# Kernel tuning notes

Hardware: AMD Instinct MI355X
Metric: run time of the kernel (lower is better)

Reference implementation:

```python
import jax, jax.numpy as jnp
import numpy as np

N = 100000   # nodes
E = 1600000  # edges (avg degree 16)
F_IN, F_HID, F_OUT = 64, 64, 16


def setup_inputs() -> dict:
    key = jax.random.key(0)
    ks = jax.random.split(key, 10)
    features = jax.random.normal(ks[0], (N, F_IN), dtype=jnp.float32)
    src = jax.random.randint(ks[1], (E,), 0, N, dtype=jnp.int32)
    dst = jax.random.randint(ks[2], (E,), 0, N, dtype=jnp.int32)
    # Xavier-uniform weights, zero bias (matches nn.init in the module)
    def xavier(k, fan_in, fan_out):
        lim = np.sqrt(6.0 / (fan_in + fan_out))
        return jax.random.uniform(k, (fan_in, fan_out), jnp.float32, -lim, lim)
    return {
        "features": features,
        "W1": xavier(ks[3], F_IN, F_HID), "b1": jnp.zeros((F_HID,), jnp.float32),
        "W2": xavier(ks[4], F_HID, F_HID), "b2": jnp.zeros((F_HID,), jnp.float32),
        "W3": xavier(ks[5], F_HID, F_OUT), "b3": jnp.zeros((F_OUT,), jnp.float32),
        "src": src, "dst": dst,
    }


def pairnorm_scs(x):
    # PairNorm 'PN-SCS', scale=1
    col_mean = x.mean(axis=0)                                    # [F]
    rownorm = jnp.sqrt(1e-6 + jnp.sum(x * x, axis=1, keepdims=True))  # [N,1]
    return x / rownorm - col_mean


def graph_conv(h, src, dst, W, b):
    # copy_u('h','m') + sum reduce over edges, plus self-loop
    agg = jax.ops.segment_sum(h[src], dst, num_segments=N) + h   # [N,F]
    return agg @ W + b


def reference(features, W1, b1, W2, b2, W3, b3, src, dst):
    h = features
    for W, b in ((W1, b1), (W2, b2)):
        h = pairnorm_scs(h)
        h = jax.nn.relu(graph_conv(h, src, dst, W, b))
        # dropout p=0.0 -> identity
    return graph_conv(h, src, dst, W3, b3)
```

## Files before the change

### kernel.cpp

```cpp
#include <hip/hip_runtime.h>
#include <hip/hip_fp8.h>


#define NHB 128

typedef float floatx2 __attribute__((ext_vector_type(2)));

__device__ __forceinline__ unsigned short f2bf(float f) {
  unsigned u = __builtin_bit_cast(unsigned, f);
  u += 0x7FFFu + ((u >> 16) & 1u);
  return (unsigned short)(u >> 16);
}
__device__ __forceinline__ float bf2f(unsigned short h) {
  return __builtin_bit_cast(float, ((unsigned)h) << 16);
}
__device__ __forceinline__ float rlane(float v, int k) {
  return __builtin_bit_cast(
      float, __builtin_amdgcn_readlane(__builtin_bit_cast(int, v), k));
}
__device__ __forceinline__ unsigned char f2fp8(float f) {
  __hip_fp8_e4m3 t(f);
  return (unsigned char)t.__x;
}
__device__ __forceinline__ float fp8tof(unsigned v) {
#if __has_builtin(__builtin_amdgcn_cvt_f32_fp8)
  return __builtin_amdgcn_cvt_f32_fp8((int)v, 0);
#else
  const unsigned h = ((v << 8) & 0x8000u) | ((v << 7) & 0x3f80u);
  __half_raw hr; hr.x = (unsigned short)h;
  return (float)__half(hr) * 256.0f;
#endif
}
__device__ __forceinline__ floatx2 fp8x2tof(unsigned short p) {
#if __has_builtin(__builtin_amdgcn_cvt_pk_f32_fp8)
  return __builtin_amdgcn_cvt_pk_f32_fp8((int)(unsigned)p, false);
#else
  floatx2 r; r.x = fp8tof(p & 0xffu); r.y = fp8tof(p >> 8); return r;
#endif
}

__global__ __launch_bounds__(256) void prelude_kernel(
    const int* __restrict__ dst, int* __restrict__ cntA, int E,
    const float* __restrict__ x, float* __restrict__ cs, int n4) {
  __shared__ int lc[NHB];
  __shared__ float lds[16][64];
  const int t = threadIdx.x;
  if (t < NHB) lc[t] = 0;
  __syncthreads();
  const int stride = gridDim.x * blockDim.x;
  for (int e = blockIdx.x * blockDim.x + t; e < E; e += stride)
    atomicAdd(&lc[__builtin_nontemporal_load(&dst[e]) >> 10], 1);

  float s0 = 0.f, s1 = 0.f, s2 = 0.f, s3 = 0.f;
  for (int i = blockIdx.x * blockDim.x + t; i < n4; i += stride) {
    float4 v = ((const float4*)x)[i];
    s0 += v.x; s1 += v.y; s2 += v.z; s3 += v.w;
  }
  const int r = t >> 4;
  const int cq = (t & 15) * 4;
  lds[r][cq + 0] = s0; lds[r][cq + 1] = s1; lds[r][cq + 2] = s2; lds[r][cq + 3] = s3;
  __syncthreads();
  if (t < NHB && lc[t]) atomicAdd(&cntA[t], lc[t]);
  if (t < 64) {
    float tot = 0.f;
    #pragma unroll
    for (int rr = 0; rr < 16; ++rr) tot += lds[rr][t];
    unsafeAtomicAdd(&cs[t], tot);
  }
}

__global__ __launch_bounds__(256) void matnorm_kernel(
    const float* x, const float* __restrict__ W,
    const float* __restrict__ cs, unsigned char* __restrict__ z,
    int N, float invN) {
  const int lane = threadIdx.x & 63;
  const int wid  = blockIdx.x * (blockDim.x >> 6) + (threadIdx.x >> 6);
  const int nw   = gridDim.x * (blockDim.x >> 6);

  float w[64];
  float cm0 = 0.f, cm1 = 0.f, cm2 = 0.f, cm3 = 0.f;
  #pragma unroll
  for (int k = 0; k < 64; k += 4) {
    w[k + 0] = W[(k + 0) * 64 + lane];
    w[k + 1] = W[(k + 1) * 64 + lane];
    w[k + 2] = W[(k + 2) * 64 + lane];
    w[k + 3] = W[(k + 3) * 64 + lane];
    cm0 = fmaf(cs[k + 0], w[k + 0], cm0);
    cm1 = fmaf(cs[k + 1], w[k + 1], cm1);
    cm2 = fmaf(cs[k + 2], w[k + 2], cm2);
    cm3 = fmaf(cs[k + 3], w[k + 3], cm3);
  }
  const float cm = ((cm0 + cm1) + (cm2 + cm3)) * invN;

  for (int row = wid; row < N; row += nw) {
    const float xv = x[(size_t)row * 64 + lane];
    float ss = xv * xv;
    #pragma unroll
    for (int m = 1; m < 64; m <<= 1) ss += __shfl_xor(ss, m, 64);
    const float rinv = 1.0f / sqrtf(1e-6f + ss);
    float a0 = 0.f, a1 = 0.f, a2 = 0.f, a3 = 0.f;
    #pragma unroll
    for (int k = 0; k < 64; k += 4) {
      a0 = fmaf(rlane(xv, k + 0), w[k + 0], a0);
      a1 = fmaf(rlane(xv, k + 1), w[k + 1], a1);
      a2 = fmaf(rlane(xv, k + 2), w[k + 2], a2);
      a3 = fmaf(rlane(xv, k + 3), w[k + 3], a3);
    }
    const float acc = (a0 + a1) + (a2 + a3);
    z[(size_t)row * 64 + lane] = f2fp8(acc * rinv - cm);
  }
}

__global__ __launch_bounds__(256) void matnorm2_kernel(
    const float* x, const float* __restrict__ W,
    float* __restrict__ cs, unsigned char* __restrict__ z, int N) {
  __shared__ float lred[4][64];
  const int lane = threadIdx.x & 63;
  const int wv   = threadIdx.x >> 6;
  const int wid  = blockIdx.x * (blockDim.x >> 6) + wv;
  const int nw   = gridDim.x * (blockDim.x >> 6);

  float w[64];
  #pragma unroll
  for (int k = 0; k < 64; k += 4) {
    w[k + 0] = W[(k + 0) * 64 + lane];
    w[k + 1] = W[(k + 1) * 64 + lane];
    w[k + 2] = W[(k + 2) * 64 + lane];
    w[k + 3] = W[(k + 3) * 64 + lane];
  }

  float csum = 0.f;
  for (int row = wid; row < N; row += nw) {
    const float xv = x[(size_t)row * 64 + lane];
    csum += xv;
    float ss = xv * xv;
    #pragma unroll
    for (int m = 1; m < 64; m <<= 1) ss += __shfl_xor(ss, m, 64);
    const float rinv = 1.0f / sqrtf(1e-6f + ss);
    float a0 = 0.f, a1 = 0.f, a2 = 0.f, a3 = 0.f;
    #pragma unroll
    for (int k = 0; k < 64; k += 4) {
      a0 = fmaf(rlane(xv, k + 0), w[k + 0], a0);
      a1 = fmaf(rlane(xv, k + 1), w[k + 1], a1);
      a2 = fmaf(rlane(xv, k + 2), w[k + 2], a2);
      a3 = fmaf(rlane(xv, k + 3), w[k + 3], a3);
    }
    const float acc = (a0 + a1) + (a2 + a3);
    z[(size_t)row * 64 + lane] = f2fp8(acc * rinv);
  }
  lred[wv][lane] = csum;
  __syncthreads();
  if (threadIdx.x < 64) {
    const float tot = lred[0][lane] + lred[1][lane] + lred[2][lane] + lred[3][lane];
    unsafeAtomicAdd(&cs[lane], tot);
  }
}

__global__ void cm2_kernel(const float* __restrict__ cs,
                           const float* __restrict__ W,
                           float* __restrict__ cm2, float invN) {
  const int m = threadIdx.x;
  float a0 = 0.f, a1 = 0.f, a2 = 0.f, a3 = 0.f;
  #pragma unroll
  for (int k = 0; k < 64; k += 4) {
    a0 = fmaf(cs[k + 0], W[(k + 0) * 64 + m], a0);
    a1 = fmaf(cs[k + 1], W[(k + 1) * 64 + m], a1);
    a2 = fmaf(cs[k + 2], W[(k + 2) * 64 + m], a2);
    a3 = fmaf(cs[k + 3], W[(k + 3) * 64 + m], a3);
  }
  cm2[m] = ((a0 + a1) + (a2 + a3)) * invN;
}


__global__ void scanA_kernel(const int* __restrict__ cntA,
                             int* __restrict__ baseA, int* __restrict__ curA,
                             int NHI) {
  __shared__ int s[NHB];
  const int t = threadIdx.x;
  const int v = (t < NHI) ? cntA[t] : 0;
  s[t] = v;
  __syncthreads();
  int acc = v;
  for (int off = 1; off < NHB; off <<= 1) {
    const int add = (t >= off) ? s[t - off] : 0;
    __syncthreads();
    acc += add;
    s[t] = acc;
    __syncthreads();
  }
  const int excl = acc - v;
  if (t < NHI) { baseA[t] = excl; curA[t] = excl; }
  if (t == NHI - 1) baseA[NHI] = acc;
}

#define TILE 2048
#define CAPA 48
__global__ __launch_bounds__(256) void scatterA_kernel(
    const int* __restrict__ src, const int* __restrict__ dst,
    int* __restrict__ curA, unsigned* __restrict__ ppack, int E) {
  __shared__ unsigned lpk[NHB][CAPA];
  __shared__ int lcnt[NHB], lbase[NHB];
  const int t = threadIdx.x;
  if (t < NHB) lcnt[t] = 0;
  __syncthreads();
  const int ntiles = (E + TILE - 1) / TILE;
  for (int tile = blockIdx.x; tile < ntiles; tile += gridDim.x) {
    const int base = tile * TILE;
    #pragma unroll
    for (int j = 0; j < TILE / 256; ++j) {
      const int e = base + j * 256 + t;
      if (e < E) {
        const int d = __builtin_nontemporal_load(&dst[e]);
        const int s = __builtin_nontemporal_load(&src[e]);
        const unsigned pw = ((unsigned)s << 10) | ((unsigned)d & 1023u);
        const int p = d >> 10;
        const int slot = atomicAdd(&lcnt[p], 1);
        if (slot < CAPA) lpk[p][slot] = pw;
        else ppack[atomicAdd(&curA[p], 1)] = pw;
      }
    }
    __syncthreads();
    if (t < NHB) {
      int c = lcnt[t]; if (c > CAPA) c = CAPA;
      lbase[t] = c ? atomicAdd(&curA[t], c) : 0;
      lcnt[t] = c;
    }
    __syncthreads();
    for (int p = 0; p < NHB; ++p) {
      const int c = lcnt[p];
      if (t < c) ppack[lbase[p] + t] = lpk[p][t];
    }
    __syncthreads();
    if (t < NHB) lcnt[t] = 0;
    __syncthreads();
  }
}

__global__ __launch_bounds__(1024) void fillsort_kernel(
    const unsigned* __restrict__ ppack, const int* __restrict__ baseA,
    int* __restrict__ rowstart, int* __restrict__ csr, int N, int E) {
  __shared__ int hist[1024];
  __shared__ int bs[1024];
  const int t = threadIdx.x;
  const int h = blockIdx.x;
  const int nlo = h << 10;
  const int elo = baseA[h], ehi = baseA[h + 1];

  hist[t] = 0;
  __syncthreads();

  int e = elo + t;
  for (; e + 3 * 1024 < ehi; e += 4 * 1024) {
    const unsigned p0 = ppack[e], p1 = ppack[e + 1024],
                   p2 = ppack[e + 2048], p3 = ppack[e + 3072];
    atomicAdd(&hist[p0 & 1023u], 1); atomicAdd(&hist[p1 & 1023u], 1);
    atomicAdd(&hist[p2 & 1023u], 1); atomicAdd(&hist[p3 & 1023u], 1);
  }
  for (; e < ehi; e += 1024) atomicAdd(&hist[ppack[e] & 1023u], 1);
  __syncthreads();

  const int c = hist[t];
  bs[t] = c;
  __syncthreads();
  for (int off = 1; off < 1024; off <<= 1) {
    const int v = (t >= off) ? bs[t - off] : 0;
    __syncthreads();
    bs[t] += v;
    __syncthreads();
  }
  const int excl = bs[t] - c;

  hist[t] = excl;
  const int n0 = nlo + t;
  if (n0 < N) rowstart[n0] = elo + excl;
  if (h == 0 && t == 0) rowstart[N] = E;
  __syncthreads();

  e = elo + t;
  for (; e + 3 * 1024 < ehi; e += 4 * 1024) {
    const unsigned p0 = ppack[e],        p1 = ppack[e + 1024];
    const unsigned p2 = ppack[e + 2048], p3 = ppack[e + 3072];
    csr[elo + atomicAdd(&hist[p0 & 1023u], 1)] = (int)(p0 >> 10);
    csr[elo + atomicAdd(&hist[p1 & 1023u], 1)] = (int)(p1 >> 10);
    csr[elo + atomicAdd(&hist[p2 & 1023u], 1)] = (int)(p2 >> 10);
    csr[elo + atomicAdd(&hist[p3 & 1023u], 1)] = (int)(p3 >> 10);
  }
  for (; e < ehi; e += 1024) {
    const unsigned p = ppack[e];
    csr[elo + atomicAdd(&hist[p & 1023u], 1)] = (int)(p >> 10);
  }
}

__global__ __launch_bounds__(256) void gather64_kernel(
    const unsigned char* __restrict__ z, const float* __restrict__ b,
    const int* __restrict__ rowstart, const int* __restrict__ csr,
    float* __restrict__ agg, int N) {
  const int lane = threadIdx.x & 63;
  const int h    = lane >> 5;
  const int il   = lane & 31;
  const int f0   = il << 1;
  const int pair = blockIdx.x * (blockDim.x >> 6) + (threadIdx.x >> 6);
  const int n0 = pair << 1;
  if (n0 >= N) return;
  const int node = n0 + h;
  const bool hv = (node < N);
  const int start = hv ? rowstart[node] : 0;
  const int end   = hv ? rowstart[node + 1] : 0;
  const int deg   = end - start;
  const int degA = __builtin_amdgcn_readfirstlane(deg);
  const int degB = __builtin_amdgcn_readlane(deg, 32);
  const int maxdeg = degA > degB ? degA : degB;

  const unsigned char* zp = z + f0;
  const unsigned short sv =
      hv ? *(const unsigned short*)(zp + (size_t)node * 64) : (unsigned short)0;

  float a00 = 0.f, a01 = 0.f, a10 = 0.f, a11 = 0.f;
  for (int w0 = 0; w0 < maxdeg; w0 += 32) {
    const int ei = start + w0 + il;
    const int safe = (ei < end) ? ei : (end > start ? end - 1 : 0);
    const int cidx = csr[safe];
    const int rem = maxdeg - w0;
    const int nloc = rem < 32 ? rem : 32;
    int j0 = 0;
    for (; j0 + 16 <= nloc; j0 += 16) {
      int idx[16];
      #pragma unroll
      for (int j = 0; j < 16; ++j)
        idx[j] = __shfl(cidx, (h << 5) + j0 + j, 64);
      unsigned short hh[16];
      #pragma unroll
      for (int j = 0; j < 16; ++j)
        hh[j] = *(const unsigned short*)(zp + (size_t)(unsigned)idx[j] * 64u);
      #pragma unroll
      for (int j = 0; j < 16; ++j) {
        const unsigned short m = (w0 + j0 + j < deg) ? hh[j] : (unsigned short)0;
        const floatx2 v = fp8x2tof(m);
        if (j & 1) { a10 += v.x; a11 += v.y; }
        else       { a00 += v.x; a01 += v.y; }
      }
    }
    for (; j0 + 4 <= nloc; j0 += 4) {
      int idx[4];
      #pragma unroll
      for (int j = 0; j < 4; ++j)
        idx[j] = __shfl(cidx, (h << 5) + j0 + j, 64);
      unsigned short hh[4];
      #pragma unroll
      for (int j = 0; j < 4; ++j)
        hh[j] = *(const unsigned short*)(zp + (size_t)(unsigned)idx[j] * 64u);
      #pragma unroll
      for (int j = 0; j < 4; ++j) {
        const unsigned short m = (w0 + j0 + j < deg) ? hh[j] : (unsigned short)0;
        const floatx2 v = fp8x2tof(m);
        if (j & 1) { a10 += v.x; a11 += v.y; }
        else       { a00 += v.x; a01 += v.y; }
      }
    }
    for (; j0 < nloc; ++j0) {
      const int idx = __shfl(cidx, (h << 5) + j0, 64);
      const unsigned short hh =
          *(const unsigned short*)(zp + (size_t)(unsigned)idx * 64u);
      const unsigned short m = (w0 + j0 < deg) ? hh : (unsigned short)0;
      const floatx2 v = fp8x2tof(m);
      a00 += v.x; a01 += v.y;
    }
  }
  if (hv) {
    const floatx2 sf = fp8x2tof(sv);
    const float2 bb = *(const float2*)(b + f0);
    float2 st;
    st.x = fmaxf(sf.x + bb.x + a00 + a10, 0.f);
    st.y = fmaxf(sf.y + bb.y + a01 + a11, 0.f);
    *(float2*)(agg + (size_t)node * 64 + f0) = st;
  }
}

__global__ __launch_bounds__(256) void gather_l2_kernel(
    const unsigned char* __restrict__ z2, const float* __restrict__ b2,
    const float* __restrict__ W3, const float* __restrict__ cm2,
    const int* __restrict__ rowstart, const int* __restrict__ csr,
    unsigned char* __restrict__ z3, int N) {
  const int lane = threadIdx.x & 63;
  int node = blockIdx.x * (blockDim.x >> 6) + (threadIdx.x >> 6);
  if (node >= N) return;
  node = __builtin_amdgcn_readfirstlane(node);
  float4 w4[4];
  #pragma unroll
  for (int q = 0; q < 4; ++q)
    w4[q] = ((const float4*)(W3 + lane * 16))[q];
  const float cml = cm2[lane];

  const int start = rowstart[node];
  const int end   = rowstart[node + 1];
  const unsigned char hs = z2[(size_t)node * 64 + lane];
  float a0 = 0.f, a1 = 0.f, a2 = 0.f, a3 = 0.f;
  int e = start;
  for (; e + 16 <= end; e += 16) {
    unsigned char h[16];
    #pragma unroll
    for (int j = 0; j < 16; ++j) h[j] = z2[(size_t)csr[e + j] * 64 + lane];
    #pragma unroll
    for (int j = 0; j < 16; j += 4) {
      a0 += fp8tof(h[j + 0]); a1 += fp8tof(h[j + 1]);
      a2 += fp8tof(h[j + 2]); a3 += fp8tof(h[j + 3]);
    }
  }
  for (; e + 4 <= end; e += 4) {
    unsigned char h[4];
    #pragma unroll
    for (int j = 0; j < 4; ++j) h[j] = z2[(size_t)csr[e + j] * 64 + lane];
    a0 += fp8tof(h[0]); a1 += fp8tof(h[1]); a2 += fp8tof(h[2]); a3 += fp8tof(h[3]);
  }
  for (; e < end; ++e) a0 += fp8tof(z2[(size_t)csr[e] * 64 + lane]);
  const float sum = (a0 + a1) + (a2 + a3);
  const float corr = (float)(end - start + 1) * cml;
  const float o = fmaxf(fp8tof(hs) + b2[lane] + sum - corr, 0.f);

  float p[16];
  #pragma unroll
  for (int q = 0; q < 4; ++q) {
    p[4 * q + 0] = o * w4[q].x;
    p[4 * q + 1] = o * w4[q].y;
    p[4 * q + 2] = o * w4[q].z;
    p[4 * q + 3] = o * w4[q].w;
  }
  {
    const bool up = (lane & 1);
    #pragma unroll
    for (int m = 0; m < 8; ++m) {
      const float mine = up ? p[m + 8] : p[m];
      const float give = up ? p[m] : p[m + 8];
      p[m] = mine + __shfl_xor(give, 1, 64);
    }
  }
  {
    const bool up = (lane & 2);
    #pragma unroll
    for (int m = 0; m < 4; ++m) {
      const float mine = up ? p[m + 4] : p[m];
      const float give = up ? p[m] : p[m + 4];
      p[m] = mine + __shfl_xor(give, 2, 64);
    }
  }
  {
    const bool up = (lane & 4);
    #pragma unroll
    for (int m = 0; m < 2; ++m) {
      const float mine = up ? p[m + 2] : p[m];
      const float give = up ? p[m] : p[m + 2];
      p[m] = mine + __shfl_xor(give, 4, 64);
    }
  }
  {
    const bool up = (lane & 8);
    const float mine = up ? p[1] : p[0];
    const float give = up ? p[0] : p[1];
    p[0] = mine + __shfl_xor(give, 8, 64);
  }
  p[0] += __shfl_xor(p[0], 16, 64);
  p[0] += __shfl_xor(p[0], 32, 64);

  if (lane < 16) {
    const int j = ((lane & 1) << 3) | ((lane & 2) << 1) |
                  ((lane & 4) >> 1) | ((lane & 8) >> 3);
    z3[(size_t)node * 16 + j] = f2fp8(p[0]);
  }
}

__global__ __launch_bounds__(256) void gather16_kernel(
    const unsigned char* __restrict__ z3, const float* __restrict__ b3,
    const int* __restrict__ rowstart, const int* __restrict__ csr,
    float* __restrict__ out, int N) {
  const int lane = threadIdx.x & 63;
  const int f = lane & 15;
  const int g = lane >> 4;
  int node = blockIdx.x * (blockDim.x >> 6) + (threadIdx.x >> 6);
  if (node >= N) return;
  node = __builtin_amdgcn_readfirstlane(node);
  const int start = rowstart[node];
  const int end   = rowstart[node + 1];
  float acc0 = 0.f, acc1 = 0.f;
  int e = start + g;
  for (; e + 4 < end; e += 8) {
    acc0 += fp8tof(z3[(size_t)csr[e] * 16 + f]);
    acc1 += fp8tof(z3[(size_t)csr[e + 4] * 16 + f]);
  }
  if (e < end) acc0 += fp8tof(z3[(size_t)csr[e] * 16 + f]);
  float acc = acc0 + acc1;
  acc += __shfl_xor(acc, 16, 64);
  acc += __shfl_xor(acc, 32, 64);
  if (lane < 16)
    out[(size_t)node * 16 + f] = fp8tof(z3[(size_t)node * 16 + f]) + b3[f] + acc;
}

extern "C" void kernel_launch(void* const* d_in, const int* in_sizes, int n_in,
                              void* d_out, int out_size, void* d_ws, size_t ws_size,
                              hipStream_t stream) {
  const float* feat = (const float*)d_in[0];
  const float* W1 = (const float*)d_in[1];
  const float* b1 = (const float*)d_in[2];
  const float* W2 = (const float*)d_in[3];
  const float* b2 = (const float*)d_in[4];
  const float* W3 = (const float*)d_in[5];
  const float* b3 = (const float*)d_in[6];
  const int* src = (const int*)d_in[7];
  const int* dst = (const int*)d_in[8];
  const int N = in_sizes[0] / 64;
  const int E = in_sizes[7];
  float* out = (float*)d_out;

  float* B            = (float*)d_ws;
  unsigned char* zb   = (unsigned char*)(B + (size_t)N * 64);
  unsigned char* z3b  = zb + (size_t)N * 64;
  int* cntA  = (int*)(z3b + (size_t)N * 16);
  float* cs1 = (float*)(cntA + NHB);
  float* cs2 = cs1 + 64;
  float* cm2w = cs2 + 64;
  int* baseA    = (int*)(cm2w + 64);
  int* curA     = baseA + NHB + 1;
  int* rowstart = curA + NHB;
  int* csr      = rowstart + N + 1;
  unsigned* ppack = (unsigned*)zb;

  const int NHI = (N + 1023) >> 10;
  const int node_blocks = (N + 3) / 4;
  const int npairs = (N + 1) / 2;
  const int pair_blocks = (npairs + 3) / 4;
  const float invN = 1.0f / (float)N;

  hipMemsetAsync(cntA, 0, (NHB + 128) * sizeof(int), stream);
  prelude_kernel<<<512, 256, 0, stream>>>(dst, cntA, E, feat, cs1, N * 16);
  scanA_kernel<<<1, NHB, 0, stream>>>(cntA, baseA, curA, NHI);
  scatterA_kernel<<<512, 256, 0, stream>>>(src, dst, curA, ppack, E);
  fillsort_kernel<<<NHI, 1024, 0, stream>>>(ppack, baseA, rowstart, csr, N, E);

  matnorm_kernel<<<1024, 256, 0, stream>>>(feat, W1, cs1, zb, N, invN);
  gather64_kernel<<<pair_blocks, 256, 0, stream>>>(zb, b1, rowstart, csr, B, N);

  matnorm2_kernel<<<1024, 256, 0, stream>>>(B, W2, cs2, zb, N);
  cm2_kernel<<<1, 64, 0, stream>>>(cs2, W2, cm2w, invN);
  gather_l2_kernel<<<node_blocks, 256, 0, stream>>>(zb, b2, W3, cm2w, rowstart,
                                                    csr, z3b, N);

  gather16_kernel<<<node_blocks, 256, 0, stream>>>(z3b, b3, rowstart, csr, out, N);
}
```

Measured before the change: 371.6 us.

## Replace bucketed two-pass CSR build with per-node degree count, scan, atomic scatter

The CSR construction used to bucket edges into 1024-node groups, stage them in LDS, then do a per-bucket local sort. It is replaced by per-node global atomic degree counting, a single-block scan over N, and a direct atomic scatter into CSR. This removes one kernel and the packed intermediate buffer. In exchange it relies on 1.6M scattered global atomics and uses a single-block serial scan. The order of neighbours within a row also becomes nondeterministic.

```diff
diff --git a/kernel.cpp b/kernel.cpp
--- a/kernel.cpp
+++ b/kernel.cpp
@@ -2,18 +2,8 @@
 #include <hip/hip_fp8.h>
 
 
-#define NHB 128
-
 typedef float floatx2 __attribute__((ext_vector_type(2)));
 
-__device__ __forceinline__ unsigned short f2bf(float f) {
-  unsigned u = __builtin_bit_cast(unsigned, f);
-  u += 0x7FFFu + ((u >> 16) & 1u);
-  return (unsigned short)(u >> 16);
-}
-__device__ __forceinline__ float bf2f(unsigned short h) {
-  return __builtin_bit_cast(float, ((unsigned)h) << 16);
-}
 __device__ __forceinline__ float rlane(float v, int k) {
   return __builtin_bit_cast(
       float, __builtin_amdgcn_readlane(__builtin_bit_cast(int, v), k));
@@ -40,16 +30,13 @@
 }
 
 __global__ __launch_bounds__(256) void prelude_kernel(
-    const int* __restrict__ dst, int* __restrict__ cntA, int E,
+    const int* __restrict__ dst, int* __restrict__ deg, int E,
     const float* __restrict__ x, float* __restrict__ cs, int n4) {
-  __shared__ int lc[NHB];
   __shared__ float lds[16][64];
   const int t = threadIdx.x;
-  if (t < NHB) lc[t] = 0;
-  __syncthreads();
   const int stride = gridDim.x * blockDim.x;
   for (int e = blockIdx.x * blockDim.x + t; e < E; e += stride)
-    atomicAdd(&lc[__builtin_nontemporal_load(&dst[e]) >> 10], 1);
+    atomicAdd(&deg[__builtin_nontemporal_load(&dst[e])], 1);
 
   float s0 = 0.f, s1 = 0.f, s2 = 0.f, s3 = 0.f;
   for (int i = blockIdx.x * blockDim.x + t; i < n4; i += stride) {
@@ -60,12 +47,49 @@
   const int cq = (t & 15) * 4;
   lds[r][cq + 0] = s0; lds[r][cq + 1] = s1; lds[r][cq + 2] = s2; lds[r][cq + 3] = s3;
   __syncthreads();
-  if (t < NHB && lc[t]) atomicAdd(&cntA[t], lc[t]);
   if (t < 64) {
     float tot = 0.f;
     #pragma unroll
     for (int rr = 0; rr < 16; ++rr) tot += lds[rr][t];
     unsafeAtomicAdd(&cs[t], tot);
+  }
+}
+
+__global__ __launch_bounds__(1024) void scanN_kernel(
+    const int* __restrict__ deg, int* __restrict__ rowstart,
+    int* __restrict__ cur, int N) {
+  __shared__ int bs[1024];
+  const int t = threadIdx.x;
+  const int per = (N + 1023) >> 10;
+  const int lo = t * per;
+  const int hi = (lo + per < N) ? (lo + per) : N;
+  int s = 0;
+  for (int i = lo; i < hi; ++i) s += deg[i];
+  bs[t] = s;
+  __syncthreads();
+  int acc = s;
+  for (int off = 1; off < 1024; off <<= 1) {
+    const int add = (t >= off) ? bs[t - off] : 0;
+    __syncthreads();
+    acc += add;
+    bs[t] = acc;
+    __syncthreads();
+  }
+  int run = acc - s;
+  for (int i = lo; i < hi; ++i) {
+    rowstart[i] = run; cur[i] = run; run += deg[i];
+  }
+  if (t == 1023) rowstart[N] = run;
+}
+
+__global__ __launch_bounds__(256) void scatter_kernel(
+    const int* __restrict__ src, const int* __restrict__ dst,
+    int* __restrict__ cur, int* __restrict__ csr, int E) {
+  const int stride = gridDim.x * blockDim.x;
+  for (int e = blockIdx.x * blockDim.x + threadIdx.x; e < E; e += stride) {
+    const int d = __builtin_nontemporal_load(&dst[e]);
+    const int s = __builtin_nontemporal_load(&src[e]);
+    csr[atomicAdd(&cur[d], 1)] = s;
   }
 }
 
@@ -169,126 +193,6 @@
     a3 = fmaf(cs[k + 3], W[(k + 3) * 64 + m], a3);
   }
   cm2[m] = ((a0 + a1) + (a2 + a3)) * invN;
-}
-
-
-__global__ void scanA_kernel(const int* __restrict__ cntA,
-                             int* __restrict__ baseA, int* __restrict__ curA,
-                             int NHI) {
-  __shared__ int s[NHB];
-  const int t = threadIdx.x;
-  const int v = (t < NHI) ? cntA[t] : 0;
-  s[t] = v;
-  __syncthreads();
-  int acc = v;
-  for (int off = 1; off < NHB; off <<= 1) {
-    const int add = (t >= off) ? s[t - off] : 0;
-    __syncthreads();
-    acc += add;
-    s[t] = acc;
-    __syncthreads();
-  }
-  const int excl = acc - v;
-  if (t < NHI) { baseA[t] = excl; curA[t] = excl; }
-  if (t == NHI - 1) baseA[NHI] = acc;
-}
-
-#define TILE 2048
-#define CAPA 48
-__global__ __launch_bounds__(256) void scatterA_kernel(
-    const int* __restrict__ src, const int* __restrict__ dst,
-    int* __restrict__ curA, unsigned* __restrict__ ppack, int E) {
-  __shared__ unsigned lpk[NHB][CAPA];
-  __shared__ int lcnt[NHB], lbase[NHB];
-  const int t = threadIdx.x;
-  if (t < NHB) lcnt[t] = 0;
-  __syncthreads();
-  const int ntiles = (E + TILE - 1) / TILE;
-  for (int tile = blockIdx.x; tile < ntiles; tile += gridDim.x) {
-    const int base = tile * TILE;
-    #pragma unroll
-    for (int j = 0; j < TILE / 256; ++j) {
-      const int e = base + j * 256 + t;
-      if (e < E) {
-        const int d = __builtin_nontemporal_load(&dst[e]);
-        const int s = __builtin_nontemporal_load(&src[e]);
-        const unsigned pw = ((unsigned)s << 10) | ((unsigned)d & 1023u);
-        const int p = d >> 10;
-        const int slot = atomicAdd(&lcnt[p], 1);
-        if (slot < CAPA) lpk[p][slot] = pw;
-        else ppack[atomicAdd(&curA[p], 1)] = pw;
-      }
-    }
-    __syncthreads();
-    if (t < NHB) {
-      int c = lcnt[t]; if (c > CAPA) c = CAPA;
-      lbase[t] = c ? atomicAdd(&curA[t], c) : 0;
-      lcnt[t] = c;
-    }
-    __syncthreads();
-    for (int p = 0; p < NHB; ++p) {
-      const int c = lcnt[p];
-      if (t < c) ppack[lbase[p] + t] = lpk[p][t];
-    }
-    __syncthreads();
-    if (t < NHB) lcnt[t] = 0;
-    __syncthreads();
-  }
-}
-
-__global__ __launch_bounds__(1024) void fillsort_kernel(
-    const unsigned* __restrict__ ppack, const int* __restrict__ baseA,
-    int* __restrict__ rowstart, int* __restrict__ csr, int N, int E) {
-  __shared__ int hist[1024];
-  __shared__ int bs[1024];
-  const int t = threadIdx.x;
-  const int h = blockIdx.x;
-  const int nlo = h << 10;
-  const int elo = baseA[h], ehi = baseA[h + 1];
-
-  hist[t] = 0;
-  __syncthreads();
-
-  int e = elo + t;
-  for (; e + 3 * 1024 < ehi; e += 4 * 1024) {
-    const unsigned p0 = ppack[e], p1 = ppack[e + 1024],
-                   p2 = ppack[e + 2048], p3 = ppack[e + 3072];
-    atomicAdd(&hist[p0 & 1023u], 1); atomicAdd(&hist[p1 & 1023u], 1);
-    atomicAdd(&hist[p2 & 1023u], 1); atomicAdd(&hist[p3 & 1023u], 1);
-  }
-  for (; e < ehi; e += 1024) atomicAdd(&hist[ppack[e] & 1023u], 1);
-  __syncthreads();
-
-  const int c = hist[t];
-  bs[t] = c;
-  __syncthreads();
-  for (int off = 1; off < 1024; off <<= 1) {
-    const int v = (t >= off) ? bs[t - off] : 0;
-    __syncthreads();
-    bs[t] += v;
-    __syncthreads();
-  }
-  const int excl = bs[t] - c;
-
-  hist[t] = excl;
-  const int n0 = nlo + t;
-  if (n0 < N) rowstart[n0] = elo + excl;
-  if (h == 0 && t == 0) rowstart[N] = E;
-  __syncthreads();
-
-  e = elo + t;
-  for (; e + 3 * 1024 < ehi; e += 4 * 1024) {
-    const unsigned p0 = ppack[e],        p1 = ppack[e + 1024];
-    const unsigned p2 = ppack[e + 2048], p3 = ppack[e + 3072];
-    csr[elo + atomicAdd(&hist[p0 & 1023u], 1)] = (int)(p0 >> 10);
-    csr[elo + atomicAdd(&hist[p1 & 1023u], 1)] = (int)(p1 >> 10);
-    csr[elo + atomicAdd(&hist[p2 & 1023u], 1)] = (int)(p2 >> 10);
-    csr[elo + atomicAdd(&hist[p3 & 1023u], 1)] = (int)(p3 >> 10);
-  }
-  for (; e < ehi; e += 1024) {
-    const unsigned p = ppack[e];
-    csr[elo + atomicAdd(&hist[p & 1023u], 1)] = (int)(p >> 10);
-  }
 }
 
 __global__ __launch_bounds__(256) void gather64_kernel(
@@ -513,27 +417,24 @@
   float* B            = (float*)d_ws;
   unsigned char* zb   = (unsigned char*)(B + (size_t)N * 64);
   unsigned char* z3b  = zb + (size_t)N * 64;
-  int* cntA  = (int*)(z3b + (size_t)N * 16);
-  float* cs1 = (float*)(cntA + NHB);
+  float* cs1 = (float*)(z3b + (size_t)N * 16);
   float* cs2 = cs1 + 64;
   float* cm2w = cs2 + 64;
-  int* baseA    = (int*)(cm2w + 64);
-  int* curA     = baseA + NHB + 1;
-  int* rowstart = curA + NHB;
+  int* rowstart = (int*)(cm2w + 64);
   int* csr      = rowstart + N + 1;
-  unsigned* ppack = (unsigned*)zb;
-
-  const int NHI = (N + 1023) >> 10;
+  int* deg = (int*)zb;
+  int* cur = deg + N;
+
   const int node_blocks = (N + 3) / 4;
   const int npairs = (N + 1) / 2;
   const int pair_blocks = (npairs + 3) / 4;
   const float invN = 1.0f / (float)N;
 
-  hipMemsetAsync(cntA, 0, (NHB + 128) * sizeof(int), stream);
-  prelude_kernel<<<512, 256, 0, stream>>>(dst, cntA, E, feat, cs1, N * 16);
-  scanA_kernel<<<1, NHB, 0, stream>>>(cntA, baseA, curA, NHI);
-  scatterA_kernel<<<512, 256, 0, stream>>>(src, dst, curA, ppack, E);
-  fillsort_kernel<<<NHI, 1024, 0, stream>>>(ppack, baseA, rowstart, csr, N, E);
+  hipMemsetAsync(deg, 0, (size_t)N * sizeof(int), stream);
+  hipMemsetAsync(cs1, 0, 128 * sizeof(float), stream);
+  prelude_kernel<<<512, 256, 0, stream>>>(dst, deg, E, feat, cs1, N * 16);
+  scanN_kernel<<<1, 1024, 0, stream>>>(deg, rowstart, cur, N);
+  scatter_kernel<<<512, 256, 0, stream>>>(src, dst, cur, csr, E);
 
   matnorm_kernel<<<1024, 256, 0, stream>>>(feat, W1, cs1, zb, N, invN);
   gather64_kernel<<<pair_blocks, 256, 0, stream>>>(zb, b1, rowstart, csr, B, N);
```

Measured after the change: 694.1 us. +86.8%, slower.
